# Performance work log

Measured on AMD Instinct MI355X. Metric: run time of the kernel, lower is better.

Reference implementation:

```python
import jax, jax.numpy as jnp
import numpy as np

M_FEATS = 1536      # number of proposals (docstring: [M, K])
K_DIM = 128         # feature dim per docstring example
NUM_CLASSES = 16    # label vocabulary; torch.unique loop becomes a fixed class sweep


def setup_inputs() -> dict:
    key = jax.random.key(0)
    k1, k2 = jax.random.split(key)
    features = jax.random.normal(k1, (M_FEATS, K_DIM), dtype=jnp.float32)
    labels = jax.random.randint(k2, (M_FEATS,), 0, NUM_CLASSES, dtype=jnp.int32)
    # ious all ones -> keep = (ious >= 0.5) is all-True, so the boolean filter is identity
    ious = jnp.ones((M_FEATS,), dtype=jnp.float32)
    return {"features": features, "labels": labels, "ious": ious}


def reference(features, labels, ious):
    # reweight_func='none' -> coef = ones_like(ious); keep mask is all-True by construction
    coef = jnp.ones_like(ious)
    # similarity [M, M]; coef broadcasts over columns, matching `similarity * coef` in torch
    sim = jnp.matmul(features, features.T) * coef[None, :]
    m = sim.shape[0]
    eye = jnp.eye(m, dtype=sim.dtype)
    # ground set term: logdet(similarity + 0.5 I)  (mask_ground is all ones)
    ground = jnp.linalg.slogdet(sim + 0.5 * eye)[1]

    # Per-label logdet of the submatrix S_c + 0.5 I_{n_c}. Instead of extracting a
    # variable-size submatrix (not jit-able), embed it in a full [M, M] matrix that is
    # block-diagonal: class block = S_c + 0.5 I, off-class diagonal = 1. Its logdet
    # equals logdet(S_c + 0.5 I). Absent classes give identity -> logdet 0, matching
    # torch.unique skipping them.
    onehot = (labels[:, None] == jnp.arange(NUM_CLASSES, dtype=labels.dtype)[None, :])
    onehot = onehot.astype(sim.dtype)  # [M, C]

    def class_logdet(mask):  # mask: [M] 0/1 indicator for one class
        A = sim * (mask[:, None] * mask[None, :]) + jnp.diag(0.5 * mask + (1.0 - mask))
        return jnp.linalg.slogdet(A)[1]

    per_class = jax.vmap(class_logdet)(onehot.T)  # [C]
    loss = jnp.sum(per_class) - ground
    return loss  # scalar; .mean() of a scalar is itself
```

## Files before the change

### kernel.cpp

```cpp
#include <hip/hip_runtime.h>
#include <math.h>


#define M_FEATS 1536
#define K_DIM 128
#define NUM_CLASSES 16
#define GRAM_ELEMS (K_DIM * K_DIM)
#define SENT 0x13579BDF
#define MP 104
#define WS2 40

typedef short bf16x8 __attribute__((ext_vector_type(8)));
typedef float f32x4 __attribute__((ext_vector_type(4)));

__device__ __forceinline__ short f2bf(float x) {
    unsigned u = __float_as_uint(x);
    u += 0x7FFFu + ((u >> 16) & 1u);
    return (short)(u >> 16);
}

__device__ __forceinline__ float chol128_acc(
    const int t,
    f32x4 a00, f32x4 a01, f32x4 a02, f32x4 a03,
    f32x4 a04, f32x4 a05, f32x4 a06, f32x4 a07,
    f32x4 a10, f32x4 a11, f32x4 a12, f32x4 a13,
    f32x4 a14, f32x4 a15, f32x4 a16, f32x4 a17,
    float* __restrict__ strip, short* __restrict__ Whl, float* __restrict__ logp)
{
    const int wave = t >> 6, lane = t & 63, ln = lane & 15, quad = lane >> 4;

#pragma unroll 1
    for (int s = 0; s < 16; ++s) {
        const int k = 8 * s;

        const int sb = s >> 1, sw = sb >> 1, sx = sb & 1, sq = (s & 1) * 2;
        if (wave == sw && (quad == sq || quad == sq + 1)) {
            float* sp = strip + (quad - sq) * 4 + ln * 8;
            if (sx == 0) {
                *(f32x4*)(sp + 0)   = a00; *(f32x4*)(sp + 128) = a01;
                *(f32x4*)(sp + 256) = a02; *(f32x4*)(sp + 384) = a03;
                *(f32x4*)(sp + 512) = a04; *(f32x4*)(sp + 640) = a05;
                *(f32x4*)(sp + 768) = a06; *(f32x4*)(sp + 896) = a07;
            } else {
                *(f32x4*)(sp + 0)   = a10; *(f32x4*)(sp + 128) = a11;
                *(f32x4*)(sp + 256) = a12; *(f32x4*)(sp + 384) = a13;
                *(f32x4*)(sp + 512) = a14; *(f32x4*)(sp + 640) = a15;
                *(f32x4*)(sp + 768) = a16; *(f32x4*)(sp + 896) = a17;
            }
        }
        __syncthreads();

        if (t < K_DIM) {
            float D[8][8];
#pragma unroll
            for (int c = 0; c < 8; ++c) {
                float4 d0 = *(const float4*)(strip + (k + c) * 8);
                float4 d1 = *(const float4*)(strip + (k + c) * 8 + 4);
                D[0][c] = d0.x; D[1][c] = d0.y; D[2][c] = d0.z; D[3][c] = d0.w;
                D[4][c] = d1.x; D[5][c] = d1.y; D[6][c] = d1.z; D[7][c] = d1.w;
            }
            float4 av0 = *(const float4*)(strip + t * 8);
            float4 av1 = *(const float4*)(strip + t * 8 + 4);
            float a[8] = {av0.x, av0.y, av0.z, av0.w, av1.x, av1.y, av1.z, av1.w};

            float L[8][8], ic[8];
            float prod = 1.0f;
#pragma unroll
            for (int c = 0; c < 8; ++c) {
                float v = D[c][c];
#pragma unroll
                for (int m = 0; m < c; ++m) v = fmaf(-L[c][m], L[c][m], v);
                prod *= v;
                ic[c] = rsqrtf(v);
#pragma unroll
                for (int r = c + 1; r < 8; ++r) {
                    float x = D[r][c];
#pragma unroll
                    for (int m = 0; m < c; ++m) x = fmaf(-L[r][m], L[c][m], x);
                    L[r][c] = x * ic[c];
                }
            }
            if (t == 0) logp[s] = prod;

            float w[8];
#pragma unroll
            for (int c = 0; c < 8; ++c) {
                float x = a[c];
#pragma unroll
                for (int m = 0; m < c; ++m) x = fmaf(-L[c][m], w[m], x);
                w[c] = x * ic[c];
            }
            if (t < k) {
#pragma unroll
                for (int c = 0; c < 8; ++c) w[c] = 0.f;
            }

            unsigned uh[4], ul[4];
#pragma unroll
            for (int j = 0; j < 4; ++j) {
                const float w0 = w[2 * j], w1 = w[2 * j + 1];
                const unsigned h0 = (unsigned short)f2bf(w0);
                const unsigned h1 = (unsigned short)f2bf(w1);
                const float f0 = __uint_as_float(h0 << 16);
                const float f1 = __uint_as_float(h1 << 16);
                const unsigned l0 = (unsigned short)f2bf(w0 - f0);
                const unsigned l1 = (unsigned short)f2bf(w1 - f1);
                uh[j] = (h1 << 16) | h0;
                ul[j] = (l1 << 16) | l0;
            }
            short* wp = Whl + t * WS2;
            *(int4*)(wp) = make_int4((int)uh[0], (int)uh[1], (int)uh[2], (int)uh[3]);
            *(int4*)(wp + 8) = make_int4((int)ul[0], (int)ul[1], (int)ul[2], (int)ul[3]);
            *(int4*)(wp + 16) = make_int4((int)(uh[0] ^ 0x80008000u), (int)(uh[1] ^ 0x80008000u),
                                          (int)(uh[2] ^ 0x80008000u), (int)(uh[3] ^ 0x80008000u));
            *(int4*)(wp + 24) = make_int4((int)(ul[0] ^ 0x80008000u), (int)(ul[1] ^ 0x80008000u),
                                          (int)(ul[2] ^ 0x80008000u), (int)(ul[3] ^ 0x80008000u));
        }
        __syncthreads();

        const int live = 8 * (s + 1);
        const bool live0 = ((wave * 2 + 0) * 16 + 16) > live;
        const bool live1 = ((wave * 2 + 1) * 16 + 16) > live;
        if (live0 | live1) {
            const bf16x8 z = {};
            bf16x8 fa0 = *(const bf16x8*)(Whl + (((wave * 2 + 0) * 16 + ln) * WS2) + (quad & 1) * 8);
            bf16x8 fa1 = *(const bf16x8*)(Whl + (((wave * 2 + 1) * 16 + ln) * WS2) + (quad & 1) * 8);
            fa0 = (quad < 2) ? fa0 : z;
            fa1 = (quad < 2) ? fa1 : z;
#define TRAIL_TC(TC) \
            if ((TC * 16 + 16) > live) { \
                const short* bp = Whl + (TC * 16 + ln) * WS2; \
                bf16x8 bh = *(const bf16x8*)(bp + 16); \
                bf16x8 bl = *(const bf16x8*)(bp + 24); \
                bh = (quad < 2) ? bh : z; \
                bl = (quad < 2) ? bl : z; \
                if (live0) { \
                    a0##TC = __builtin_amdgcn_mfma_f32_16x16x32_bf16(fa0, bh, a0##TC, 0, 0, 0); \
                    a0##TC = __builtin_amdgcn_mfma_f32_16x16x32_bf16(fa0, bl, a0##TC, 0, 0, 0); \
                } \
                if (live1) { \
                    a1##TC = __builtin_amdgcn_mfma_f32_16x16x32_bf16(fa1, bh, a1##TC, 0, 0, 0); \
                    a1##TC = __builtin_amdgcn_mfma_f32_16x16x32_bf16(fa1, bl, a1##TC, 0, 0, 0); \
                } \
            }
            TRAIL_TC(0) TRAIL_TC(1) TRAIL_TC(2) TRAIL_TC(3)
            TRAIL_TC(4) TRAIL_TC(5) TRAIL_TC(6) TRAIL_TC(7)
#undef TRAIL_TC
        }
    }

    float ls = 0.0f;
    if (t == 0) {
#pragma unroll
        for (int ss = 0; ss < 16; ++ss) ls += logf(logp[ss]);
    }
    return ls;
}

__global__ __launch_bounds__(256, 1) void fused_kernel(
    const float* __restrict__ f, const int* __restrict__ labels,
    float* __restrict__ groundG, float* __restrict__ ldet,
    int* __restrict__ flagG, int* __restrict__ flag3,
    float* __restrict__ out)
{
    __shared__ int cnt;
    __shared__ int list[M_FEATS];
    __shared__ __align__(16) short FT[K_DIM * MP];
    __shared__ __align__(16) float strip[8 * 128];
    __shared__ __align__(16) short Whl[K_DIM * WS2];
    __shared__ float logp[16];

    const int b = blockIdx.x;
    const int t = threadIdx.x;
    const int wave = t >> 6, lane = t & 63, ln = lane & 15, quad = lane >> 4;

#define DECL16(P) \
    f32x4 P##00 = (f32x4){0.f,0.f,0.f,0.f}, P##01 = (f32x4){0.f,0.f,0.f,0.f}, \
          P##02 = (f32x4){0.f,0.f,0.f,0.f}, P##03 = (f32x4){0.f,0.f,0.f,0.f}, \
          P##04 = (f32x4){0.f,0.f,0.f,0.f}, P##05 = (f32x4){0.f,0.f,0.f,0.f}, \
          P##06 = (f32x4){0.f,0.f,0.f,0.f}, P##07 = (f32x4){0.f,0.f,0.f,0.f}, \
          P##10 = (f32x4){0.f,0.f,0.f,0.f}, P##11 = (f32x4){0.f,0.f,0.f,0.f}, \
          P##12 = (f32x4){0.f,0.f,0.f,0.f}, P##13 = (f32x4){0.f,0.f,0.f,0.f}, \
          P##14 = (f32x4){0.f,0.f,0.f,0.f}, P##15 = (f32x4){0.f,0.f,0.f,0.f}, \
          P##16 = (f32x4){0.f,0.f,0.f,0.f}, P##17 = (f32x4){0.f,0.f,0.f,0.f}
#define FOR16(OP) \
    OP(g00,0,0) OP(g01,0,1) OP(g02,0,2) OP(g03,0,3) \
    OP(g04,0,4) OP(g05,0,5) OP(g06,0,6) OP(g07,0,7) \
    OP(g10,1,0) OP(g11,1,1) OP(g12,1,2) OP(g13,1,3) \
    OP(g14,1,4) OP(g15,1,5) OP(g16,1,6) OP(g17,1,7)
#define DIAGADD(VAR, X, TC) \
    if ((wave * 2 + X) == TC) { \
        if (ln == quad * 4 + 0) VAR[0] += 0.5f; \
        else if (ln == quad * 4 + 1) VAR[1] += 0.5f; \
        else if (ln == quad * 4 + 2) VAR[2] += 0.5f; \
        else if (ln == quad * 4 + 3) VAR[3] += 0.5f; }

    if (b < NUM_CLASSES) {
        const int cls = b;
        if (t == 0) cnt = 0;
        __syncthreads();
        {
            const unsigned long long ltmask = (lane == 63)
                ? 0x7FFFFFFFFFFFFFFFull : ((1ull << lane) - 1ull);
#pragma unroll
            for (int it = 0; it < M_FEATS / 256; ++it) {
                const int i = it * 256 + t;
                const bool pred = (labels[i] == cls);
                const unsigned long long mask = __ballot(pred);
                int base = 0;
                if (lane == 0 && mask)
                    base = atomicAdd(&cnt, __popcll(mask));
                base = __shfl(base, 0);
                if (pred)
                    list[base + __popcll(mask & ltmask)] = i;
            }
        }
        __syncthreads();
        const int n = cnt;

        DECL16(g);

        const int mlane = t & 31, cgrp = t >> 5;
        const int nchunks = (n + 95) / 96;
        for (int ch = 0; ch < nchunks; ++ch) {
            const int cb = ch * 96;
#pragma unroll
            for (int it = 0; it < 12; ++it) {
                const int m = (it % 3) * 32 + mlane;
                const int cgp = (it / 3) * 8 + cgrp;
                const int gm = cb + m;
                float4 v = make_float4(0.f, 0.f, 0.f, 0.f);
                if (gm < n) {
                    const int src = list[gm];
                    v = *(const float4*)(f + (size_t)src * K_DIM + cgp * 4);
                }
                FT[(cgp * 4 + 0) * MP + m] = f2bf(v.x);
                FT[(cgp * 4 + 1) * MP + m] = f2bf(v.y);
                FT[(cgp * 4 + 2) * MP + m] = f2bf(v.z);
                FT[(cgp * 4 + 3) * MP + m] = f2bf(v.w);
            }
            __syncthreads();
#pragma unroll
            for (int kc = 0; kc < 3; ++kc) {
                const int kb = kc * 32 + quad * 8;
                const bf16x8 fa0 = *(const bf16x8*)(FT + ((wave * 2 + 0) * 16 + ln) * MP + kb);
                const bf16x8 fa1 = *(const bf16x8*)(FT + ((wave * 2 + 1) * 16 + ln) * MP + kb);
#define GRAM_TC(TC) { \
                const bf16x8 bb = *(const bf16x8*)(FT + (TC * 16 + ln) * MP + kb); \
                g0##TC = __builtin_amdgcn_mfma_f32_16x16x32_bf16(fa0, bb, g0##TC, 0, 0, 0); \
                g1##TC = __builtin_amdgcn_mfma_f32_16x16x32_bf16(fa1, bb, g1##TC, 0, 0, 0); }
                GRAM_TC(0) GRAM_TC(1) GRAM_TC(2) GRAM_TC(3)
                GRAM_TC(4) GRAM_TC(5) GRAM_TC(6) GRAM_TC(7)
#undef GRAM_TC
            }
            __syncthreads();
        }

#define SCAT(VAR, X, TC) { \
        const int row0 = (wave * 2 + X) * 16 + quad * 4; \
        const int col = TC * 16 + ln; \
        unsafeAtomicAdd(&groundG[(row0 + 0) * K_DIM + col], VAR[0]); \
        unsafeAtomicAdd(&groundG[(row0 + 1) * K_DIM + col], VAR[1]); \
        unsafeAtomicAdd(&groundG[(row0 + 2) * K_DIM + col], VAR[2]); \
        unsafeAtomicAdd(&groundG[(row0 + 3) * K_DIM + col], VAR[3]); }
        FOR16(SCAT)
#undef SCAT
        __syncthreads();
        if (t == 0)
            __hip_atomic_store(&flagG[cls], SENT, __ATOMIC_RELEASE,
                               __HIP_MEMORY_SCOPE_AGENT);

        FOR16(DIAGADD)

        float ls = chol128_acc(t,
            g00, g01, g02, g03, g04, g05, g06, g07,
            g10, g11, g12, g13, g14, g15, g16, g17,
            strip, Whl, logp);

        if (t == 0) {
            ldet[cls] = ls;
            __hip_atomic_store(&flag3[cls], SENT, __ATOMIC_RELEASE,
                               __HIP_MEMORY_SCOPE_AGENT);
        }
        return;
    }

    if (t < NUM_CLASSES)
        while (__hip_atomic_load(&flagG[t], __ATOMIC_ACQUIRE,
                                 __HIP_MEMORY_SCOPE_AGENT) != SENT)
            __builtin_amdgcn_s_sleep(2);
    __syncthreads();

    DECL16(g);
#define LOADG(VAR, X, TC) { \
    const int row0 = (wave * 2 + X) * 16 + quad * 4; \
    const int col = TC * 16 + ln; \
    VAR = (f32x4){groundG[(row0 + 0) * K_DIM + col], \
                  groundG[(row0 + 1) * K_DIM + col], \
                  groundG[(row0 + 2) * K_DIM + col], \
                  groundG[(row0 + 3) * K_DIM + col]}; }
    FOR16(LOADG)
#undef LOADG
    FOR16(DIAGADD)

    float ls = chol128_acc(t,
        g00, g01, g02, g03, g04, g05, g06, g07,
        g10, g11, g12, g13, g14, g15, g16, g17,
        strip, Whl, logp);

    if (t < NUM_CLASSES)
        while (__hip_atomic_load(&flag3[t], __ATOMIC_ACQUIRE,
                                 __HIP_MEMORY_SCOPE_AGENT) != SENT)
            __builtin_amdgcn_s_sleep(2);
    __syncthreads();

    if (t == 0) {
        float total = 1920.0f * 0.6931471805599453f - ls;
#pragma unroll
        for (int c = 0; c < NUM_CLASSES; ++c) total += ldet[c];
        out[0] = total;
    }
}

extern "C" void kernel_launch(void* const* d_in, const int* in_sizes, int n_in,
                              void* d_out, int out_size, void* d_ws, size_t ws_size,
                              hipStream_t stream)
{
    const float* features = (const float*)d_in[0];
    const int* labels = (const int*)d_in[1];

    float* groundG = (float*)d_ws;
    float* ldetp   = groundG + GRAM_ELEMS;
    int* flagG     = (int*)(ldetp + NUM_CLASSES);
    int* flag3     = flagG + NUM_CLASSES;

    fused_kernel<<<NUM_CLASSES + 1, 256, 0, stream>>>(
        features, labels, groundG, ldetp, flagG, flag3, (float*)d_out);
}
```

Baseline: 96.71 us.

## Double block to 512 threads with one 16-row tile per wave

Changes the block from 4 to 8 waves, so each wave owns one 16-row strip of the 128x128 Gram/Cholesky matrix instead of two. Accumulator registers per thread are halved and the MFMA work in the Gram and trailing-update loops is spread over more waves. The Gram chunk loop also skips k-chunks beyond the live row count in the last partial chunk. The cost is more waves taking part in each of the many per-step __syncthreads in the serial Cholesky loop.

```diff
diff --git a/kernel.cpp b/kernel.cpp
--- a/kernel.cpp
+++ b/kernel.cpp
@@ -21,10 +21,8 @@
 
 __device__ __forceinline__ float chol128_acc(
     const int t,
-    f32x4 a00, f32x4 a01, f32x4 a02, f32x4 a03,
-    f32x4 a04, f32x4 a05, f32x4 a06, f32x4 a07,
-    f32x4 a10, f32x4 a11, f32x4 a12, f32x4 a13,
-    f32x4 a14, f32x4 a15, f32x4 a16, f32x4 a17,
+    f32x4 a0, f32x4 a1, f32x4 a2, f32x4 a3,
+    f32x4 a4, f32x4 a5, f32x4 a6, f32x4 a7,
     float* __restrict__ strip, short* __restrict__ Whl, float* __restrict__ logp)
 {
     const int wave = t >> 6, lane = t & 63, ln = lane & 15, quad = lane >> 4;
@@ -33,20 +31,13 @@
     for (int s = 0; s < 16; ++s) {
         const int k = 8 * s;
 
-        const int sb = s >> 1, sw = sb >> 1, sx = sb & 1, sq = (s & 1) * 2;
+        const int sw = s >> 1, sq = (s & 1) * 2;
         if (wave == sw && (quad == sq || quad == sq + 1)) {
             float* sp = strip + (quad - sq) * 4 + ln * 8;
-            if (sx == 0) {
-                *(f32x4*)(sp + 0)   = a00; *(f32x4*)(sp + 128) = a01;
-                *(f32x4*)(sp + 256) = a02; *(f32x4*)(sp + 384) = a03;
-                *(f32x4*)(sp + 512) = a04; *(f32x4*)(sp + 640) = a05;
-                *(f32x4*)(sp + 768) = a06; *(f32x4*)(sp + 896) = a07;
-            } else {
-                *(f32x4*)(sp + 0)   = a10; *(f32x4*)(sp + 128) = a11;
-                *(f32x4*)(sp + 256) = a12; *(f32x4*)(sp + 384) = a13;
-                *(f32x4*)(sp + 512) = a14; *(f32x4*)(sp + 640) = a15;
-                *(f32x4*)(sp + 768) = a16; *(f32x4*)(sp + 896) = a17;
-            }
+            *(f32x4*)(sp + 0)   = a0; *(f32x4*)(sp + 128) = a1;
+            *(f32x4*)(sp + 256) = a2; *(f32x4*)(sp + 384) = a3;
+            *(f32x4*)(sp + 512) = a4; *(f32x4*)(sp + 640) = a5;
+            *(f32x4*)(sp + 768) = a6; *(f32x4*)(sp + 896) = a7;
         }
         __syncthreads();
 
@@ -119,14 +110,10 @@
         __syncthreads();
 
         const int live = 8 * (s + 1);
-        const bool live0 = ((wave * 2 + 0) * 16 + 16) > live;
-        const bool live1 = ((wave * 2 + 1) * 16 + 16) > live;
-        if (live0 | live1) {
+        if ((wave * 16 + 16) > live) {
             const bf16x8 z = {};
-            bf16x8 fa0 = *(const bf16x8*)(Whl + (((wave * 2 + 0) * 16 + ln) * WS2) + (quad & 1) * 8);
-            bf16x8 fa1 = *(const bf16x8*)(Whl + (((wave * 2 + 1) * 16 + ln) * WS2) + (quad & 1) * 8);
-            fa0 = (quad < 2) ? fa0 : z;
-            fa1 = (quad < 2) ? fa1 : z;
+            bf16x8 fa = *(const bf16x8*)(Whl + ((wave * 16 + ln) * WS2) + (quad & 1) * 8);
+            fa = (quad < 2) ? fa : z;
 #define TRAIL_TC(TC) \
             if ((TC * 16 + 16) > live) { \
                 const short* bp = Whl + (TC * 16 + ln) * WS2; \
@@ -134,14 +121,8 @@
                 bf16x8 bl = *(const bf16x8*)(bp + 24); \
                 bh = (quad < 2) ? bh : z; \
                 bl = (quad < 2) ? bl : z; \
-                if (live0) { \
-                    a0##TC = __builtin_amdgcn_mfma_f32_16x16x32_bf16(fa0, bh, a0##TC, 0, 0, 0); \
-                    a0##TC = __builtin_amdgcn_mfma_f32_16x16x32_bf16(fa0, bl, a0##TC, 0, 0, 0); \
-                } \
-                if (live1) { \
-                    a1##TC = __builtin_amdgcn_mfma_f32_16x16x32_bf16(fa1, bh, a1##TC, 0, 0, 0); \
-                    a1##TC = __builtin_amdgcn_mfma_f32_16x16x32_bf16(fa1, bl, a1##TC, 0, 0, 0); \
-                } \
+                a##TC = __builtin_amdgcn_mfma_f32_16x16x32_bf16(fa, bh, a##TC, 0, 0, 0); \
+                a##TC = __builtin_amdgcn_mfma_f32_16x16x32_bf16(fa, bl, a##TC, 0, 0, 0); \
             }
             TRAIL_TC(0) TRAIL_TC(1) TRAIL_TC(2) TRAIL_TC(3)
             TRAIL_TC(4) TRAIL_TC(5) TRAIL_TC(6) TRAIL_TC(7)
@@ -157,7 +138,7 @@
     return ls;
 }
 
-__global__ __launch_bounds__(256, 1) void fused_kernel(
+__global__ __launch_bounds__(512, 1) void fused_kernel(
     const float* __restrict__ f, const int* __restrict__ labels,
     float* __restrict__ groundG, float* __restrict__ ldet,
     int* __restrict__ flagG, int* __restrict__ flag3,
@@ -174,22 +155,14 @@
     const int t = threadIdx.x;
     const int wave = t >> 6, lane = t & 63, ln = lane & 15, quad = lane >> 4;
 
-#define DECL16(P) \
-    f32x4 P##00 = (f32x4){0.f,0.f,0.f,0.f}, P##01 = (f32x4){0.f,0.f,0.f,0.f}, \
-          P##02 = (f32x4){0.f,0.f,0.f,0.f}, P##03 = (f32x4){0.f,0.f,0.f,0.f}, \
-          P##04 = (f32x4){0.f,0.f,0.f,0.f}, P##05 = (f32x4){0.f,0.f,0.f,0.f}, \
-          P##06 = (f32x4){0.f,0.f,0.f,0.f}, P##07 = (f32x4){0.f,0.f,0.f,0.f}, \
-          P##10 = (f32x4){0.f,0.f,0.f,0.f}, P##11 = (f32x4){0.f,0.f,0.f,0.f}, \
-          P##12 = (f32x4){0.f,0.f,0.f,0.f}, P##13 = (f32x4){0.f,0.f,0.f,0.f}, \
-          P##14 = (f32x4){0.f,0.f,0.f,0.f}, P##15 = (f32x4){0.f,0.f,0.f,0.f}, \
-          P##16 = (f32x4){0.f,0.f,0.f,0.f}, P##17 = (f32x4){0.f,0.f,0.f,0.f}
-#define FOR16(OP) \
-    OP(g00,0,0) OP(g01,0,1) OP(g02,0,2) OP(g03,0,3) \
-    OP(g04,0,4) OP(g05,0,5) OP(g06,0,6) OP(g07,0,7) \
-    OP(g10,1,0) OP(g11,1,1) OP(g12,1,2) OP(g13,1,3) \
-    OP(g14,1,4) OP(g15,1,5) OP(g16,1,6) OP(g17,1,7)
-#define DIAGADD(VAR, X, TC) \
-    if ((wave * 2 + X) == TC) { \
+#define DECL8(P) \
+    f32x4 P##0 = (f32x4){0.f,0.f,0.f,0.f}, P##1 = (f32x4){0.f,0.f,0.f,0.f}, \
+          P##2 = (f32x4){0.f,0.f,0.f,0.f}, P##3 = (f32x4){0.f,0.f,0.f,0.f}, \
+          P##4 = (f32x4){0.f,0.f,0.f,0.f}, P##5 = (f32x4){0.f,0.f,0.f,0.f}, \
+          P##6 = (f32x4){0.f,0.f,0.f,0.f}, P##7 = (f32x4){0.f,0.f,0.f,0.f}
+#define FOR8(OP) OP(g0,0) OP(g1,1) OP(g2,2) OP(g3,3) OP(g4,4) OP(g5,5) OP(g6,6) OP(g7,7)
+#define DIAGADD(VAR, TC) \
+    if (wave == TC) { \
         if (ln == quad * 4 + 0) VAR[0] += 0.5f; \
         else if (ln == quad * 4 + 1) VAR[1] += 0.5f; \
         else if (ln == quad * 4 + 2) VAR[2] += 0.5f; \
@@ -203,8 +176,8 @@
             const unsigned long long ltmask = (lane == 63)
                 ? 0x7FFFFFFFFFFFFFFFull : ((1ull << lane) - 1ull);
 #pragma unroll
-            for (int it = 0; it < M_FEATS / 256; ++it) {
-                const int i = it * 256 + t;
+            for (int it = 0; it < M_FEATS / 512; ++it) {
+                const int i = it * 512 + t;
                 const bool pred = (labels[i] == cls);
                 const unsigned long long mask = __ballot(pred);
                 int base = 0;
@@ -218,16 +191,20 @@
         __syncthreads();
         const int n = cnt;
 
-        DECL16(g);
+        DECL8(g);
 
         const int mlane = t & 31, cgrp = t >> 5;
         const int nchunks = (n + 95) / 96;
         for (int ch = 0; ch < nchunks; ++ch) {
             const int cb = ch * 96;
-#pragma unroll
-            for (int it = 0; it < 12; ++it) {
-                const int m = (it % 3) * 32 + mlane;
-                const int cgp = (it / 3) * 8 + cgrp;
+            const int live = n - cb;
+            const int kcmax = (live >= 96) ? 3 : ((live + 31) >> 5);
+#pragma unroll
+            for (int it = 0; it < 6; ++it) {
+                const int mg = it % 3;
+                if (mg >= kcmax) continue;
+                const int m = mg * 32 + mlane;
+                const int cgp = (it / 3) * 16 + cgrp;
                 const int gm = cb + m;
                 float4 v = make_float4(0.f, 0.f, 0.f, 0.f);
                 if (gm < n) {
@@ -240,15 +217,12 @@
                 FT[(cgp * 4 + 3) * MP + m] = f2bf(v.w);
             }
             __syncthreads();
-#pragma unroll
-            for (int kc = 0; kc < 3; ++kc) {
+            for (int kc = 0; kc < kcmax; ++kc) {
                 const int kb = kc * 32 + quad * 8;
-                const bf16x8 fa0 = *(const bf16x8*)(FT + ((wave * 2 + 0) * 16 + ln) * MP + kb);
-                const bf16x8 fa1 = *(const bf16x8*)(FT + ((wave * 2 + 1) * 16 + ln) * MP + kb);
+                const bf16x8 fa = *(const bf16x8*)(FT + (wave * 16 + ln) * MP + kb);
 #define GRAM_TC(TC) { \
                 const bf16x8 bb = *(const bf16x8*)(FT + (TC * 16 + ln) * MP + kb); \
-                g0##TC = __builtin_amdgcn_mfma_f32_16x16x32_bf16(fa0, bb, g0##TC, 0, 0, 0); \
-                g1##TC = __builtin_amdgcn_mfma_f32_16x16x32_bf16(fa1, bb, g1##TC, 0, 0, 0); }
+                g##TC = __builtin_amdgcn_mfma_f32_16x16x32_bf16(fa, bb, g##TC, 0, 0, 0); }
                 GRAM_TC(0) GRAM_TC(1) GRAM_TC(2) GRAM_TC(3)
                 GRAM_TC(4) GRAM_TC(5) GRAM_TC(6) GRAM_TC(7)
 #undef GRAM_TC
@@ -256,26 +230,24 @@
             __syncthreads();
         }
 
-#define SCAT(VAR, X, TC) { \
-        const int row0 = (wave * 2 + X) * 16 + quad * 4; \
+#define SCAT(VAR, TC) { \
+        const int row0 = wave * 16 + quad * 4; \
         const int col = TC * 16 + ln; \
         unsafeAtomicAdd(&groundG[(row0 + 0) * K_DIM + col], VAR[0]); \
         unsafeAtomicAdd(&groundG[(row0 + 1) * K_DIM + col], VAR[1]); \
         unsafeAtomicAdd(&groundG[(row0 + 2) * K_DIM + col], VAR[2]); \
         unsafeAtomicAdd(&groundG[(row0 + 3) * K_DIM + col], VAR[3]); }
-        FOR16(SCAT)
+        FOR8(SCAT)
 #undef SCAT
         __syncthreads();
         if (t == 0)
             __hip_atomic_store(&flagG[cls], SENT, __ATOMIC_RELEASE,
                                __HIP_MEMORY_SCOPE_AGENT);
 
-        FOR16(DIAGADD)
-
-        float ls = chol128_acc(t,
-            g00, g01, g02, g03, g04, g05, g06, g07,
-            g10, g11, g12, g13, g14, g15, g16, g17,
-            strip, Whl, logp);
+        FOR8(DIAGADD)
+
+        float ls = chol128_acc(t, g0, g1, g2, g3, g4, g5, g6, g7,
+                               strip, Whl, logp);
 
         if (t == 0) {
             ldet[cls] = ls;
@@ -291,22 +263,20 @@
             __builtin_amdgcn_s_sleep(2);
     __syncthreads();
 
-    DECL16(g);
-#define LOADG(VAR, X, TC) { \
-    const int row0 = (wave * 2 + X) * 16 + quad * 4; \
+    DECL8(g);
+#define LOADG(VAR, TC) { \
+    const int row0 = wave * 16 + quad * 4; \
     const int col = TC * 16 + ln; \
     VAR = (f32x4){groundG[(row0 + 0) * K_DIM + col], \
                   groundG[(row0 + 1) * K_DIM + col], \
                   groundG[(row0 + 2) * K_DIM + col], \
                   groundG[(row0 + 3) * K_DIM + col]}; }
-    FOR16(LOADG)
+    FOR8(LOADG)
 #undef LOADG
-    FOR16(DIAGADD)
-
-    float ls = chol128_acc(t,
-        g00, g01, g02, g03, g04, g05, g06, g07,
-        g10, g11, g12, g13, g14, g15, g16, g17,
-        strip, Whl, logp);
+    FOR8(DIAGADD)
+
+    float ls = chol128_acc(t, g0, g1, g2, g3, g4, g5, g6, g7,
+                           strip, Whl, logp);
 
     if (t < NUM_CLASSES)
         while (__hip_atomic_load(&flag3[t], __ATOMIC_ACQUIRE,
@@ -334,6 +304,6 @@
     int* flagG     = (int*)(ldetp + NUM_CLASSES);
     int* flag3     = flagG + NUM_CLASSES;
 
-    fused_kernel<<<NUM_CLASSES + 1, 256, 0, stream>>>(
+    fused_kernel<<<NUM_CLASSES + 1, 512, 0, stream>>>(
         features, labels, groundG, ldetp, flagG, flag3, (float*)d_out);
 }
```

Result: faster. 86.54 us (-10.5%).
